# Performance work log

Hardware: AMD Instinct MI355X
Metric: run time of the kernel (lower is better)

Reference implementation:

```python
import jax, jax.numpy as jnp
import numpy as np

FEATURE_SIZE = 1000000  # padding index == FEATURE_SIZE
NEG_INF = -1e9


def _attn_pool(emb_table, hist_idx, ad_idx):
    # hist_idx: [B, L] int, ad_idx: [B] int
    hist = emb_table[hist_idx]          # [B, L, K] gather
    ad = emb_table[ad_idx]              # [B, K]
    score = jnp.einsum('blk,bk->bl', hist, ad)          # [B, L]
    score = jnp.where(hist_idx != FEATURE_SIZE, score, NEG_INF)
    w = jax.nn.softmax(score, axis=1)
    return jnp.einsum('blk,bl->bk', hist, w)            # [B, K]


def setup_inputs() -> dict:
    key = jax.random.key(0)
    ks = jax.random.split(key, 12)
    B, F, K = 4096, 8, 64
    V = FEATURE_SIZE + 1
    d_in = 3 * K + F * K  # 704
    inp = {
        'feature_idx': jax.random.randint(ks[0], (B, F), 0, FEATURE_SIZE),
        'hist_item': jax.random.randint(ks[1], (B, 350), 0, V),
        'hist_author': jax.random.randint(ks[2], (B, 250), 0, V),
        'hist_music': jax.random.randint(ks[3], (B, 100), 0, V),
        'emb_table': jax.random.normal(ks[4], (V, K), jnp.float32),
        'W1': jax.random.normal(ks[5], (d_in, 512), jnp.float32) * 0.02,
        'b1': jnp.zeros((512,), jnp.float32),
        'W2': jax.random.normal(ks[6], (512, 256), jnp.float32) * 0.02,
        'b2': jnp.zeros((256,), jnp.float32),
        'W3': jax.random.normal(ks[7], (256, 128), jnp.float32) * 0.02,
        'b3': jnp.zeros((128,), jnp.float32),
        'Wo': jax.random.normal(ks[8], (128, 1), jnp.float32) * 0.02,
        'bo': jnp.zeros((1,), jnp.float32),
    }
    return inp


def reference(feature_idx, hist_item, hist_author, hist_music, emb_table,
              W1, b1, W2, b2, W3, b3, Wo, bo):
    # ad indices for the three behavior features: columns 2, 3, 6
    pools = [
        _attn_pool(emb_table, hist_item, feature_idx[:, 2]),
        _attn_pool(emb_table, hist_author, feature_idx[:, 3]),
        _attn_pool(emb_table, hist_music, feature_idx[:, 6]),
    ]
    user_beha = jnp.concatenate(pools, axis=1)                    # [B, 3K]
    B = feature_idx.shape[0]
    ad_emb = emb_table[feature_idx].reshape(B, -1)                # [B, F*K]
    x = jnp.concatenate([user_beha, ad_emb], axis=1)              # [B, 704]
    x = jax.nn.relu(x @ W1 + b1)
    x = jax.nn.relu(x @ W2 + b2)
    x = jax.nn.relu(x @ W3 + b3)
    logits = x @ Wo + bo                                          # [B, 1]
    return logits
```

## Files before the change

kernel.cpp:

```cpp
#include <hip/hip_runtime.h>
#include <cstddef>

#define BATCH   4096
#define PAD_IDX 1000000
#define NEG_INF_F (-1e9f)

typedef __attribute__((ext_vector_type(8))) short bf16x8;
typedef __attribute__((ext_vector_type(4))) float f32x4;
typedef unsigned short u16;

__device__ __forceinline__ u16 f2bf(float f) {
    unsigned u = __float_as_uint(f);
    return (u16)((u + 0x7fffu + ((u >> 16) & 1u)) >> 16);
}
__device__ __forceinline__ float bf2f(u16 b) {
    return __uint_as_float(((unsigned)b) << 16);
}

#define UPD(mm, dd, aa, s, v)                          \
    {                                                  \
        float nm = fmaxf(mm, (s));                     \
        float sc = __expf(mm - nm);                    \
        float e  = __expf((s) - nm);                   \
        dd = fmaf(dd, sc, e);                          \
        aa.x = fmaf(aa.x, sc, e * (v).x);              \
        aa.y = fmaf(aa.y, sc, e * (v).y);              \
        aa.z = fmaf(aa.z, sc, e * (v).z);              \
        aa.w = fmaf(aa.w, sc, e * (v).w);              \
        mm = nm;                                       \
    }

#define MERGE(P)                                                  \
    {                                                             \
        float mo  = __shfl_xor(m, P);                             \
        float d_o = __shfl_xor(d, P);                             \
        float ax = __shfl_xor(acc.x, P);                          \
        float ay = __shfl_xor(acc.y, P);                          \
        float az = __shfl_xor(acc.z, P);                          \
        float aw = __shfl_xor(acc.w, P);                          \
        float nm = fmaxf(m, mo);                                  \
        float sA = __expf(m - nm), sB = __expf(mo - nm);          \
        d = d * sA + d_o * sB;                                    \
        acc.x = acc.x * sA + ax * sB;                             \
        acc.y = acc.y * sA + ay * sB;                             \
        acc.z = acc.z * sA + az * sB;                             \
        acc.w = acc.w * sA + aw * sB;                             \
        m = nm;                                                   \
    }

#define QRED(s)                       \
    s += __shfl_xor(s, 1);            \
    s += __shfl_xor(s, 2);            \
    s += __shfl_xor(s, 4);            \
    s += __shfl_xor(s, 8);

#define DOT4(v, a) ((v).x * (a).x + (v).y * (a).y + (v).z * (a).z + (v).w * (a).w)

__global__ void __launch_bounds__(256) prep_kernel(
    const int* __restrict__ fidx,
    const int* __restrict__ hist_item,
    const int* __restrict__ hist_author,
    const int* __restrict__ hist_music,
    const float* __restrict__ emb,
    const float* __restrict__ W1, const float* __restrict__ W2, const float* __restrict__ W3,
    u16* __restrict__ x,
    u16* __restrict__ w1t, u16* __restrict__ w2t, u16* __restrict__ w3t)
{
    __shared__ float tile[32][33];
    const int blk = blockIdx.x;

    if (blk < 5120) {
        const int w    = blk * 4 + (threadIdx.x >> 6);
        const int lane = threadIdx.x & 63;
        const int t16  = lane & 15;
        const int q    = lane >> 4;

        if (w < 3 * BATCH) {
            const int h = w >> 12;
            const int b = w & (BATCH - 1);
            int L, col, off;
            const int* hrow;
            if (h == 0)      { L = 350; col = 2; off = 0;   hrow = hist_item   + (size_t)b * 350; }
            else if (h == 1) { L = 250; col = 3; off = 64;  hrow = hist_author + (size_t)b * 250; }
            else             { L = 100; col = 6; off = 128; hrow = hist_music  + (size_t)b * 100; }

            const int ad_idx = fidx[b * 8 + col];
            const float4 ad4 = *(const float4*)(emb + (size_t)ad_idx * 64 + 4 * t16);

            float m = NEG_INF_F, d = 0.f;
            float4 acc = make_float4(0.f, 0.f, 0.f, 0.f);
            float mB = NEG_INF_F, dB = 0.f;
            float4 aB = make_float4(0.f, 0.f, 0.f, 0.f);

            int l = 0;
            if (L >= 16) {
                int n0 = hrow[q], n1 = hrow[4 + q], n2 = hrow[8 + q], n3 = hrow[12 + q];
                while (true) {
                    const int i0 = n0, i1 = n1, i2 = n2, i3 = n3;
                    const float4 v0 = *(const float4*)(emb + (size_t)i0 * 64 + 4 * t16);
                    const float4 v1 = *(const float4*)(emb + (size_t)i1 * 64 + 4 * t16);
                    const float4 v2 = *(const float4*)(emb + (size_t)i2 * 64 + 4 * t16);
                    const float4 v3 = *(const float4*)(emb + (size_t)i3 * 64 + 4 * t16);
                    l += 16;
                    const bool more = (l + 16 <= L);
                    if (more) {
                        n0 = hrow[l + q];      n1 = hrow[l + 4 + q];
                        n2 = hrow[l + 8 + q];  n3 = hrow[l + 12 + q];
                    }
                    float s0 = DOT4(v0, ad4);
                    float s1 = DOT4(v1, ad4);
                    float s2 = DOT4(v2, ad4);
                    float s3 = DOT4(v3, ad4);
                    QRED(s0) QRED(s1) QRED(s2) QRED(s3)
                    if (i0 == PAD_IDX) s0 = NEG_INF_F;
                    if (i1 == PAD_IDX) s1 = NEG_INF_F;
                    if (i2 == PAD_IDX) s2 = NEG_INF_F;
                    if (i3 == PAD_IDX) s3 = NEG_INF_F;
                    UPD(m, d, acc, s0, v0)
                    UPD(mB, dB, aB, s1, v1)
                    UPD(m, d, acc, s2, v2)
                    UPD(mB, dB, aB, s3, v3)
                    if (!more) break;
                }
            }
            for (; l < L; l += 4) {
                const int li = l + q;
                const int i0 = (li < L) ? hrow[li] : PAD_IDX;
                const float4 v0 = *(const float4*)(emb + (size_t)i0 * 64 + 4 * t16);
                float s0 = DOT4(v0, ad4);
                QRED(s0)
                if (i0 == PAD_IDX) s0 = NEG_INF_F;
                UPD(m, d, acc, s0, v0)
            }

            {
                float nm = fmaxf(m, mB);
                float eA = __expf(m - nm), eB = __expf(mB - nm);
                d = d * eA + dB * eB;
                acc.x = acc.x * eA + aB.x * eB;
                acc.y = acc.y * eA + aB.y * eB;
                acc.z = acc.z * eA + aB.z * eB;
                acc.w = acc.w * eA + aB.w * eB;
                m = nm;
            }
            MERGE(16)
            MERGE(32)

            if (lane < 16) {
                const float inv = 1.f / d;
                uint2 p;
                p.x = (unsigned)f2bf(acc.x * inv) | ((unsigned)f2bf(acc.y * inv) << 16);
                p.y = (unsigned)f2bf(acc.z * inv) | ((unsigned)f2bf(acc.w * inv) << 16);
                *(uint2*)(x + (size_t)b * 704 + off + 4 * t16) = p;
            }
        } else {
            const int tt = w - 3 * BATCH;
            const int b  = tt >> 1;
            const int f  = ((tt & 1) << 2) + q;
            const int idx = fidx[b * 8 + f];
            const float4 v = *(const float4*)(emb + (size_t)idx * 64 + 4 * t16);
            uint2 p;
            p.x = (unsigned)f2bf(v.x) | ((unsigned)f2bf(v.y) << 16);
            p.y = (unsigned)f2bf(v.z) | ((unsigned)f2bf(v.w) << 16);
            *(uint2*)(x + (size_t)b * 704 + 192 + (size_t)f * 64 + 4 * t16) = p;
        }
    } else {
        int t = blk - 5120;
        const float* W; u16* WT; int K, N, tk, tn;
        if (t < 352)      { W = W1; WT = w1t; K = 704; N = 512; tk = t % 22; tn = t / 22; }
        else if (t < 480) { t -= 352; W = W2; WT = w2t; K = 512; N = 256; tk = t % 16; tn = t / 16; }
        else              { t -= 480; W = W3; WT = w3t; K = 256; N = 128; tk = t % 8;  tn = t / 8;  }
        const int k0 = tk * 32, n0 = tn * 32;
        const int tx = threadIdx.x & 31, ty = threadIdx.x >> 5;
#pragma unroll
        for (int j = 0; j < 4; ++j)
            tile[ty + 8 * j][tx] = W[(size_t)(k0 + ty + 8 * j) * N + n0 + tx];
        __syncthreads();
#pragma unroll
        for (int j = 0; j < 4; ++j)
            WT[(size_t)(n0 + ty + 8 * j) * K + k0 + tx] = f2bf(tile[tx][ty + 8 * j]);
    }
}

template <int BN>
__global__ void __launch_bounds__(256) gemm_mfma(
    const u16* __restrict__ A, const u16* __restrict__ BT,
    const float* __restrict__ bias, u16* __restrict__ C,
    int M, int N, int K)
{
    constexpr int NB = BN / 16;
    __shared__ u16 As[64][40];
    __shared__ u16 Bs[BN][40];

    const int tid  = threadIdx.x;
    const int wave = tid >> 6, lane = tid & 63;
    const int quad = lane >> 4, l16 = lane & 15;
    const int bm = blockIdx.y * 64, bn = blockIdx.x * BN;

    const int srow = tid >> 2;
    const int sk   = (tid & 3) * 8;

    f32x4 acc[NB];
#pragma unroll
    for (int i = 0; i < NB; ++i) acc[i] = (f32x4){0.f, 0.f, 0.f, 0.f};

    const size_t a_base = (size_t)(bm + srow) * K + sk;

    for (int k0 = 0; k0 < K; k0 += 32) {
        *(float4*)&As[srow][sk] = *(const float4*)(A + a_base + k0);
#pragma unroll
        for (int r0 = 0; r0 < BN; r0 += 64) {
            *(float4*)&Bs[r0 + srow][sk] =
                *(const float4*)(BT + (size_t)(bn + r0 + srow) * K + k0 + sk);
        }
        __syncthreads();

        const bf16x8 af = *(const bf16x8*)&As[wave * 16 + l16][quad * 8];
#pragma unroll
        for (int ni = 0; ni < NB; ++ni) {
            const bf16x8 bf = *(const bf16x8*)&Bs[ni * 16 + l16][quad * 8];
            acc[ni] = __builtin_amdgcn_mfma_f32_16x16x32_bf16(af, bf, acc[ni], 0, 0, 0);
        }
        __syncthreads();
    }

#pragma unroll
    for (int ni = 0; ni < NB; ++ni) {
        const int col = bn + ni * 16 + l16;
        const float bv = bias[col];
#pragma unroll
        for (int r = 0; r < 4; ++r) {
            const int row = bm + wave * 16 + quad * 4 + r;
            float v = fmaxf(acc[ni][r] + bv, 0.f);
            C[(size_t)row * N + col] = f2bf(v);
        }
    }
}

__global__ void __launch_bounds__(256) gemm3_out(
    const u16* __restrict__ A, const u16* __restrict__ BT,
    const float* __restrict__ bias,
    const float* __restrict__ Wo, const float* __restrict__ bo,
    float* __restrict__ out)
{
    constexpr int K = 256, NB = 8;
    __shared__ u16 As[64][40];
    __shared__ u16 Bs[128][40];

    const int tid  = threadIdx.x;
    const int wave = tid >> 6, lane = tid & 63;
    const int quad = lane >> 4, l16 = lane & 15;
    const int bm = blockIdx.x * 64;

    const int srow = tid >> 2;
    const int sk   = (tid & 3) * 8;

    f32x4 acc[NB];
#pragma unroll
    for (int i = 0; i < NB; ++i) acc[i] = (f32x4){0.f, 0.f, 0.f, 0.f};

    const size_t a_base = (size_t)(bm + srow) * K + sk;

    for (int k0 = 0; k0 < K; k0 += 32) {
        *(float4*)&As[srow][sk] = *(const float4*)(A + a_base + k0);
#pragma unroll
        for (int r0 = 0; r0 < 128; r0 += 64) {
            *(float4*)&Bs[r0 + srow][sk] =
                *(const float4*)(BT + (size_t)(r0 + srow) * K + k0 + sk);
        }
        __syncthreads();

        const bf16x8 af = *(const bf16x8*)&As[wave * 16 + l16][quad * 8];
#pragma unroll
        for (int ni = 0; ni < NB; ++ni) {
            const bf16x8 bf = *(const bf16x8*)&Bs[ni * 16 + l16][quad * 8];
            acc[ni] = __builtin_amdgcn_mfma_f32_16x16x32_bf16(af, bf, acc[ni], 0, 0, 0);
        }
        __syncthreads();
    }

    float part[4] = {0.f, 0.f, 0.f, 0.f};
#pragma unroll
    for (int ni = 0; ni < NB; ++ni) {
        const int col = ni * 16 + l16;
        const float bv = bias[col];
        const float wv = Wo[col];
#pragma unroll
        for (int r = 0; r < 4; ++r)
            part[r] = fmaf(fmaxf(acc[ni][r] + bv, 0.f), wv, part[r]);
    }
#pragma unroll
    for (int r = 0; r < 4; ++r) {
        part[r] += __shfl_xor(part[r], 1);
        part[r] += __shfl_xor(part[r], 2);
        part[r] += __shfl_xor(part[r], 4);
        part[r] += __shfl_xor(part[r], 8);
    }
    if (l16 == 0) {
        const float b0 = bo[0];
#pragma unroll
        for (int r = 0; r < 4; ++r)
            out[bm + wave * 16 + quad * 4 + r] = part[r] + b0;
    }
}

extern "C" void kernel_launch(void* const* d_in, const int* in_sizes, int n_in,
                              void* d_out, int out_size, void* d_ws, size_t ws_size,
                              hipStream_t stream) {
    const int*   fidx  = (const int*)d_in[0];
    const int*   hitem = (const int*)d_in[1];
    const int*   hauth = (const int*)d_in[2];
    const int*   hmus  = (const int*)d_in[3];
    const float* emb   = (const float*)d_in[4];
    const float* W1 = (const float*)d_in[5];
    const float* b1 = (const float*)d_in[6];
    const float* W2 = (const float*)d_in[7];
    const float* b2 = (const float*)d_in[8];
    const float* W3 = (const float*)d_in[9];
    const float* b3 = (const float*)d_in[10];
    const float* Wo = (const float*)d_in[11];
    const float* bo = (const float*)d_in[12];
    float* out = (float*)d_out;

    u16* x   = (u16*)d_ws;
    u16* h1  = x   + (size_t)BATCH * 704;
    u16* h2  = h1  + (size_t)BATCH * 512;
    u16* w1t = h2  + (size_t)BATCH * 256;
    u16* w2t = w1t + (size_t)704 * 512;
    u16* w3t = w2t + (size_t)512 * 256;

    prep_kernel<<<5632, 256, 0, stream>>>(fidx, hitem, hauth, hmus, emb,
                                          W1, W2, W3, x, w1t, w2t, w3t);

    gemm_mfma<64><<<dim3(512 / 64, BATCH / 64), 256, 0, stream>>>(
        x, w1t, b1, h1, BATCH, 512, 704);
    gemm_mfma<64><<<dim3(256 / 64, BATCH / 64), 256, 0, stream>>>(
        h1, w2t, b2, h2, BATCH, 256, 512);
    gemm3_out<<<BATCH / 64, 256, 0, stream>>>(h2, w3t, b3, Wo, bo, out);
}
```

Measured before the change: 443.7 us.

## Double-buffer GEMM shared tiles with register prefetch and unify attention tail loop

The MLP GEMM kernels now use two shared-memory buffers, prefetching the next K-slice into registers while MFMAs run on the current slice. This cuts one barrier per iteration and hides global load latency behind compute. The attention-pool loop handles the tail by padding chunk indices with PAD_IDX, so the 4-wide unrolled body with two independent softmax accumulators covers every element instead of falling back to a scalar tail loop. In exchange, shared-memory use doubles and register pressure rises, which may lower occupancy. The padded tail also issues some gathers of the pad row.

New measurement: 441.0 us. Within noise of the previous version (-0.6%).

```diff
diff --git a/kernel.cpp b/kernel.cpp
--- a/kernel.cpp
+++ b/kernel.cpp
@@ -92,45 +92,40 @@
             float mB = NEG_INF_F, dB = 0.f;
             float4 aB = make_float4(0.f, 0.f, 0.f, 0.f);
 
-            int l = 0;
-            if (L >= 16) {
-                int n0 = hrow[q], n1 = hrow[4 + q], n2 = hrow[8 + q], n3 = hrow[12 + q];
-                while (true) {
-                    const int i0 = n0, i1 = n1, i2 = n2, i3 = n3;
-                    const float4 v0 = *(const float4*)(emb + (size_t)i0 * 64 + 4 * t16);
-                    const float4 v1 = *(const float4*)(emb + (size_t)i1 * 64 + 4 * t16);
-                    const float4 v2 = *(const float4*)(emb + (size_t)i2 * 64 + 4 * t16);
-                    const float4 v3 = *(const float4*)(emb + (size_t)i3 * 64 + 4 * t16);
-                    l += 16;
-                    const bool more = (l + 16 <= L);
-                    if (more) {
-                        n0 = hrow[l + q];      n1 = hrow[l + 4 + q];
-                        n2 = hrow[l + 8 + q];  n3 = hrow[l + 12 + q];
-                    }
-                    float s0 = DOT4(v0, ad4);
-                    float s1 = DOT4(v1, ad4);
-                    float s2 = DOT4(v2, ad4);
-                    float s3 = DOT4(v3, ad4);
-                    QRED(s0) QRED(s1) QRED(s2) QRED(s3)
-                    if (i0 == PAD_IDX) s0 = NEG_INF_F;
-                    if (i1 == PAD_IDX) s1 = NEG_INF_F;
-                    if (i2 == PAD_IDX) s2 = NEG_INF_F;
-                    if (i3 == PAD_IDX) s3 = NEG_INF_F;
-                    UPD(m, d, acc, s0, v0)
-                    UPD(mB, dB, aB, s1, v1)
-                    UPD(m, d, acc, s2, v2)
-                    UPD(mB, dB, aB, s3, v3)
-                    if (!more) break;
+            const int nC = (L + 15) >> 4;
+            int n0 = hrow[q], n1 = hrow[4 + q], n2 = hrow[8 + q], n3 = hrow[12 + q];
+            int c = 0;
+            while (true) {
+                const int i0 = n0, i1 = n1, i2 = n2, i3 = n3;
+                const float4 v0 = *(const float4*)(emb + (size_t)i0 * 64 + 4 * t16);
+                const float4 v1 = *(const float4*)(emb + (size_t)i1 * 64 + 4 * t16);
+                const float4 v2 = *(const float4*)(emb + (size_t)i2 * 64 + 4 * t16);
+                const float4 v3 = *(const float4*)(emb + (size_t)i3 * 64 + 4 * t16);
+                ++c;
+                const bool more = (c < nC);
+                if (more) {
+                    const int base = c << 4;
+                    const int e0 = base + q,      e1 = base + 4 + q;
+                    const int e2 = base + 8 + q,  e3 = base + 12 + q;
+                    n0 = (e0 < L) ? hrow[e0] : PAD_IDX;
+                    n1 = (e1 < L) ? hrow[e1] : PAD_IDX;
+                    n2 = (e2 < L) ? hrow[e2] : PAD_IDX;
+                    n3 = (e3 < L) ? hrow[e3] : PAD_IDX;
                 }
-            }
-            for (; l < L; l += 4) {
-                const int li = l + q;
-                const int i0 = (li < L) ? hrow[li] : PAD_IDX;
-                const float4 v0 = *(const float4*)(emb + (size_t)i0 * 64 + 4 * t16);
                 float s0 = DOT4(v0, ad4);
-                QRED(s0)
+                float s1 = DOT4(v1, ad4);
+                float s2 = DOT4(v2, ad4);
+                float s3 = DOT4(v3, ad4);
+                QRED(s0) QRED(s1) QRED(s2) QRED(s3)
                 if (i0 == PAD_IDX) s0 = NEG_INF_F;
+                if (i1 == PAD_IDX) s1 = NEG_INF_F;
+                if (i2 == PAD_IDX) s2 = NEG_INF_F;
+                if (i3 == PAD_IDX) s3 = NEG_INF_F;
                 UPD(m, d, acc, s0, v0)
+                UPD(mB, dB, aB, s1, v1)
+                UPD(m, d, acc, s2, v2)
+                UPD(mB, dB, aB, s3, v3)
+                if (!more) break;
             }
 
             {
@@ -189,8 +184,9 @@
     int M, int N, int K)
 {
     constexpr int NB = BN / 16;
-    __shared__ u16 As[64][40];
-    __shared__ u16 Bs[BN][40];
+    constexpr int RB = BN / 64;
+    __shared__ u16 As[2][64][40];
+    __shared__ u16 Bs[2][BN][40];
 
     const int tid  = threadIdx.x;
     const int wave = tid >> 6, lane = tid & 63;
@@ -204,24 +200,46 @@
 #pragma unroll
     for (int i = 0; i < NB; ++i) acc[i] = (f32x4){0.f, 0.f, 0.f, 0.f};
 
-    const size_t a_base = (size_t)(bm + srow) * K + sk;
-
+    const u16* aptr = A  + (size_t)(bm + srow) * K + sk;
+    const u16* bptr = BT + (size_t)(bn + srow) * K + sk;
+
+    float4 ra = *(const float4*)aptr;
+    float4 rb[RB];
+#pragma unroll
+    for (int r = 0; r < RB; ++r)
+        rb[r] = *(const float4*)(bptr + (size_t)(r * 64) * K);
+
+    *(float4*)&As[0][srow][sk] = ra;
+#pragma unroll
+    for (int r = 0; r < RB; ++r)
+        *(float4*)&Bs[0][r * 64 + srow][sk] = rb[r];
+    __syncthreads();
+
+    int cur = 0;
     for (int k0 = 0; k0 < K; k0 += 32) {
-        *(float4*)&As[srow][sk] = *(const float4*)(A + a_base + k0);
-#pragma unroll
-        for (int r0 = 0; r0 < BN; r0 += 64) {
-            *(float4*)&Bs[r0 + srow][sk] =
-                *(const float4*)(BT + (size_t)(bn + r0 + srow) * K + k0 + sk);
-        }
-        __syncthreads();
-
-        const bf16x8 af = *(const bf16x8*)&As[wave * 16 + l16][quad * 8];
+        const bool more = (k0 + 32 < K);
+        if (more) {
+            ra = *(const float4*)(aptr + k0 + 32);
+#pragma unroll
+            for (int r = 0; r < RB; ++r)
+                rb[r] = *(const float4*)(bptr + (size_t)(r * 64) * K + k0 + 32);
+        }
+
+        const bf16x8 af = *(const bf16x8*)&As[cur][wave * 16 + l16][quad * 8];
 #pragma unroll
         for (int ni = 0; ni < NB; ++ni) {
-            const bf16x8 bf = *(const bf16x8*)&Bs[ni * 16 + l16][quad * 8];
+            const bf16x8 bf = *(const bf16x8*)&Bs[cur][ni * 16 + l16][quad * 8];
             acc[ni] = __builtin_amdgcn_mfma_f32_16x16x32_bf16(af, bf, acc[ni], 0, 0, 0);
         }
-        __syncthreads();
+
+        if (more) {
+            *(float4*)&As[cur ^ 1][srow][sk] = ra;
+#pragma unroll
+            for (int r = 0; r < RB; ++r)
+                *(float4*)&Bs[cur ^ 1][r * 64 + srow][sk] = rb[r];
+            __syncthreads();
+            cur ^= 1;
+        }
     }
 
 #pragma unroll
@@ -244,8 +262,8 @@
     float* __restrict__ out)
 {
     constexpr int K = 256, NB = 8;
-    __shared__ u16 As[64][40];
-    __shared__ u16 Bs[128][40];
+    __shared__ u16 As[2][64][40];
+    __shared__ u16 Bs[2][128][40];
 
     const int tid  = threadIdx.x;
     const int wave = tid >> 6, lane = tid & 63;
@@ -259,24 +277,46 @@
 #pragma unroll
     for (int i = 0; i < NB; ++i) acc[i] = (f32x4){0.f, 0.f, 0.f, 0.f};
 
-    const size_t a_base = (size_t)(bm + srow) * K + sk;
-
+    const u16* aptr = A  + (size_t)(bm + srow) * K + sk;
+    const u16* bptr = BT + (size_t)srow * K + sk;
+
+    float4 ra = *(const float4*)aptr;
+    float4 rb[2];
+#pragma unroll
+    for (int r = 0; r < 2; ++r)
+        rb[r] = *(const float4*)(bptr + (size_t)(r * 64) * K);
+
+    *(float4*)&As[0][srow][sk] = ra;
+#pragma unroll
+    for (int r = 0; r < 2; ++r)
+        *(float4*)&Bs[0][r * 64 + srow][sk] = rb[r];
+    __syncthreads();
+
+    int cur = 0;
     for (int k0 = 0; k0 < K; k0 += 32) {
-        *(float4*)&As[srow][sk] = *(const float4*)(A + a_base + k0);
-#pragma unroll
-        for (int r0 = 0; r0 < 128; r0 += 64) {
-            *(float4*)&Bs[r0 + srow][sk] =
-                *(const float4*)(BT + (size_t)(r0 + srow) * K + k0 + sk);
-        }
-        __syncthreads();
-
-        const bf16x8 af = *(const bf16x8*)&As[wave * 16 + l16][quad * 8];
+        const bool more = (k0 + 32 < K);
+        if (more) {
+            ra = *(const float4*)(aptr + k0 + 32);
+#pragma unroll
+            for (int r = 0; r < 2; ++r)
+                rb[r] = *(const float4*)(bptr + (size_t)(r * 64) * K + k0 + 32);
+        }
+
+        const bf16x8 af = *(const bf16x8*)&As[cur][wave * 16 + l16][quad * 8];
 #pragma unroll
         for (int ni = 0; ni < NB; ++ni) {
-            const bf16x8 bf = *(const bf16x8*)&Bs[ni * 16 + l16][quad * 8];
+            const bf16x8 bf = *(const bf16x8*)&Bs[cur][ni * 16 + l16][quad * 8];
             acc[ni] = __builtin_amdgcn_mfma_f32_16x16x32_bf16(af, bf, acc[ni], 0, 0, 0);
         }
-        __syncthreads();
+
+        if (more) {
+            *(float4*)&As[cur ^ 1][srow][sk] = ra;
+#pragma unroll
+            for (int r = 0; r < 2; ++r)
+                *(float4*)&Bs[cur ^ 1][r * 64 + srow][sk] = rb[r];
+            __syncthreads();
+            cur ^= 1;
+        }
     }
 
     float part[4] = {0.f, 0.f, 0.f, 0.f};
```
